# Optimization experiments

Hardware: AMD Instinct MI355X
Metric: run time of the kernel (lower is better)

Reference implementation:

```python
import jax, jax.numpy as jnp
import numpy as np

BITS = 8
EPS = 1e-08
D_IN = 4096
D_OUT = 4096


def setup_inputs() -> dict:
    key = jax.random.key(0)
    k1, k2, k3 = jax.random.split(key, 3)
    hidden_states = jax.random.normal(k1, (4, 2048, D_IN), dtype=jnp.float32)
    # Pre-quantized (dequantized-value) weight buffer, as the module stores it in float
    qmax = 2 ** (BITS - 1) - 1
    w = jax.random.normal(k2, (D_IN, D_OUT), dtype=jnp.float32) * 0.02
    w_scale = jnp.max(jnp.abs(w)) / qmax
    weight_quantized = jnp.clip(jnp.round(w / w_scale), -qmax, qmax) * w_scale
    bias = jax.random.normal(k3, (D_OUT,), dtype=jnp.float32) * 0.01
    x_scale = jnp.asarray(3.0, dtype=jnp.float32)  # calibrated activation maxabs
    return {
        "hidden_states": hidden_states,
        "weight_quantized": weight_quantized,
        "x_scale": x_scale,
        "bias": bias,
    }


def _quantize_maxabs(x, scale, bits, eps):
    # scalar max-abs quantization with a fixed (calibrated) scale
    qmax = 2 ** (bits - 1) - 1
    step = jnp.maximum(scale, eps) / qmax
    return jnp.clip(jnp.round(x / step), -qmax, qmax) * step


def reference(hidden_states, weight_quantized, x_scale, bias):
    orig_shape = hidden_states.shape[:-1]
    d = hidden_states.shape[-1]
    x_flat = hidden_states.reshape(-1, d)
    x_q = _quantize_maxabs(x_flat, x_scale, BITS, EPS).astype(weight_quantized.dtype)
    out = x_q @ weight_quantized  # [tokens, d_out]
    out = out + bias.astype(out.dtype)[None, :]
    out = out.astype(hidden_states.dtype)
    return out.reshape(*orig_shape, weight_quantized.shape[1])
```

## Files before the change

kernel.cpp:

```cpp
#include <hip/hip_runtime.h>
#include <hip/hip_bf16.h>
#include <cstdint>

#define D_IN  4096
#define D_OUT 4096

typedef __attribute__((ext_vector_type(4)))  int   i32x4;

typedef const __attribute__((address_space(1))) unsigned g_u32;
typedef __attribute__((address_space(3))) unsigned       l_u32;

__global__ void prep_kernel(const float* __restrict__ W, int nw,
                            const float* __restrict__ x,
                            char* __restrict__ xq,
                            const float* __restrict__ xscale, int nx,
                            unsigned* __restrict__ wsp) {
    int tid = threadIdx.x;
    if (blockIdx.x < 1024) {
        __shared__ float red[256];
        float m = 0.f;
        for (int i = (blockIdx.x * 256 + tid) * 4; i < nw; i += 1024 * 256 * 4) {
            float4 v = *(const float4*)(W + i);
            m = fmaxf(m, fmaxf(fmaxf(fabsf(v.x), fabsf(v.y)),
                               fmaxf(fabsf(v.z), fabsf(v.w))));
        }
        red[tid] = m; __syncthreads();
        for (int s = 128; s > 0; s >>= 1) {
            if (tid < s) red[tid] = fmaxf(red[tid], red[tid + s]);
            __syncthreads();
        }
        if (tid == 0) atomicMax(wsp, __float_as_uint(red[0]));
    } else {
        int i = ((blockIdx.x - 1024) * 256 + tid) * 4;
        if (i >= nx) return;
        float inv = 127.0f / fmaxf(xscale[0], 1e-8f);
        float4 v = *(const float4*)(x + i);
        char4 o;
        o.x = (char)fminf(fmaxf(rintf(v.x * inv), -127.f), 127.f);
        o.y = (char)fminf(fmaxf(rintf(v.y * inv), -127.f), 127.f);
        o.z = (char)fminf(fmaxf(rintf(v.z * inv), -127.f), 127.f);
        o.w = (char)fminf(fmaxf(rintf(v.w * inv), -127.f), 127.f);
        *(char4*)(xq + i) = o;
    }
}

__global__ void convW_kernel(const float* __restrict__ W,
                             char* __restrict__ Wt,
                             const unsigned* __restrict__ wsp) {
    __shared__ float tile[64][65];
    const float wmax = __uint_as_float(wsp[0]);
    const float inv  = 127.0f / wmax;
    const int n0 = blockIdx.x * 64, k0 = blockIdx.y * 64;
    const int t = threadIdx.x;

    {
        const int r = t >> 2, c0 = (t & 3) * 16;
        const float* src = W + (size_t)(k0 + r) * D_OUT + n0 + c0;
#pragma unroll
        for (int j = 0; j < 4; ++j) {
            float4 v = *(const float4*)(src + j * 4);
            tile[r][c0 + j * 4 + 0] = v.x;
            tile[r][c0 + j * 4 + 1] = v.y;
            tile[r][c0 + j * 4 + 2] = v.z;
            tile[r][c0 + j * 4 + 3] = v.w;
        }
    }
    __syncthreads();

    {
        const int n = t >> 2, kc = (t & 3) * 16;
        int4 pk;
        int* pw = (int*)&pk;
#pragma unroll
        for (int w = 0; w < 4; ++w) {
            unsigned word = 0;
#pragma unroll
            for (int j = 0; j < 4; ++j) {
                int q = (int)rintf(tile[kc + w * 4 + j][n] * inv);
                word |= ((unsigned)(unsigned char)(char)q) << (8 * j);
            }
            pw[w] = (int)word;
        }
        *(int4*)(Wt + (size_t)(n0 + n) * D_IN + k0 + kc) = pk;
    }
}

__global__ __launch_bounds__(512, 2)
void gemm_kernel(const char* __restrict__ A,
                 const char* __restrict__ Bt,
                 const float* __restrict__ bias,
                 const float* __restrict__ xscale,
                 const unsigned* __restrict__ wsp,
                 float* __restrict__ C, int M) {
    constexpr int K = D_IN, N = D_OUT;
    constexpr int NT = K / 128;
    __shared__ char lds[2 * 65536];

    const int tid  = threadIdx.x;
    const int lane = tid & 63;
    const int wid  = tid >> 6;
    const int wr   = wid >> 2;
    const int wc   = wid & 3;

    const int nTn = N / 256;
    const int nwg = gridDim.x;
    int bid = blockIdx.x;
    int q8 = nwg >> 3, r8 = nwg & 7;
    int xcd = bid & 7, idx = bid >> 3;
    int swz = (xcd < r8 ? xcd * (q8 + 1) : r8 * (q8 + 1) + (xcd - r8) * q8) + idx;
    const int tm = swz / nTn, tn = swz % nTn;
    const int row0 = tm * 256, col0 = tn * 256;

    int srcOff[4], dstOff[4];
#pragma unroll
    for (int i = 0; i < 4; ++i) {
        int p  = (i * 512 + tid) * 16;
        int sw = p ^ (((p >> 7) & 7) << 4);
        dstOff[i] = p;
        srcOff[i] = (sw >> 7) * K + (sw & 127);
    }

    const char* srcA = A  + (size_t)row0 * K;
    const char* srcB = Bt + (size_t)col0 * K;
    char* ldsb = lds;

    auto STAGE4 = [&](const char* src, char* dst) {
#pragma unroll
        for (int i = 0; i < 4; ++i)
            __builtin_amdgcn_global_load_lds((g_u32*)(src + srcOff[i]),
                                             (l_u32*)(dst + dstOff[i]), 16, 0, 0);
    };
    auto STAGE2 = [&](const char* src, char* dst) {
#pragma unroll
        for (int i = 0; i < 2; ++i)
            __builtin_amdgcn_global_load_lds((g_u32*)(src + srcOff[i]),
                                             (l_u32*)(dst + dstOff[i]), 16, 0, 0);
    };

    STAGE2(srcB, ldsb + 32768);
    STAGE4(srcA, ldsb);
    STAGE2(srcB + 128 * K, ldsb + 32768 + 16384);
    STAGE2(srcB + 128,     ldsb + 65536 + 32768);
    STAGE4(srcA + 128,     ldsb + 65536);

    i32x4 acc[8][4];
#pragma unroll
    for (int m = 0; m < 8; ++m)
#pragma unroll
        for (int n = 0; n < 4; ++n) acc[m][n] = (i32x4){0, 0, 0, 0};

    const int cp0 = (((lane >> 4) << 4)) ^ ((lane & 7) << 4);
    const int cp1 = cp0 ^ 64;
    const int aBase = (wr * 128 + (lane & 15)) * 128;
    const int bBase = (wc * 64  + (lane & 15)) * 128;

    asm volatile("s_waitcnt vmcnt(6)" ::: "memory");

    auto KITER = [&](int t, char* cur, char* nxt) {
        i32x4 a[4][2], b01[2][2], b23[2][2];
        const char* cA = cur;
        const char* cB = cur + 32768;

        __builtin_amdgcn_s_barrier();
        if (t + 1 < NT) STAGE2(srcB + 128 * K + (t + 1) * 128, nxt + 32768 + 16384);

#pragma unroll
        for (int n = 0; n < 2; ++n) {
            b01[n][0] = *(const i32x4*)(cB + bBase + n * 2048 + cp0);
            b01[n][1] = *(const i32x4*)(cB + bBase + n * 2048 + cp1);
        }
#pragma unroll
        for (int m = 0; m < 4; ++m) {
            a[m][0] = *(const i32x4*)(cA + aBase + m * 2048 + cp0);
            a[m][1] = *(const i32x4*)(cA + aBase + m * 2048 + cp1);
        }
#pragma unroll
        for (int n = 0; n < 2; ++n) {
            b23[n][0] = *(const i32x4*)(cB + bBase + 4096 + n * 2048 + cp0);
            b23[n][1] = *(const i32x4*)(cB + bBase + 4096 + n * 2048 + cp1);
        }

        __builtin_amdgcn_s_setprio(1);
#pragma unroll
        for (int m = 0; m < 4; ++m)
#pragma unroll
            for (int n = 0; n < 2; ++n) {
                acc[m][n] = __builtin_amdgcn_mfma_i32_16x16x64_i8(a[m][0], b01[n][0], acc[m][n], 0, 0, 0);
                acc[m][n] = __builtin_amdgcn_mfma_i32_16x16x64_i8(a[m][1], b01[n][1], acc[m][n], 0, 0, 0);
            }
#pragma unroll
        for (int m = 0; m < 4; ++m)
#pragma unroll
            for (int n = 0; n < 2; ++n) {
                acc[m][n + 2] = __builtin_amdgcn_mfma_i32_16x16x64_i8(a[m][0], b23[n][0], acc[m][n + 2], 0, 0, 0);
                acc[m][n + 2] = __builtin_amdgcn_mfma_i32_16x16x64_i8(a[m][1], b23[n][1], acc[m][n + 2], 0, 0, 0);
            }
#pragma unroll
        for (int m = 0; m < 4; ++m) {
            a[m][0] = *(const i32x4*)(cA + aBase + 8192 + m * 2048 + cp0);
            a[m][1] = *(const i32x4*)(cA + aBase + 8192 + m * 2048 + cp1);
        }
#pragma unroll
        for (int m = 0; m < 4; ++m)
#pragma unroll
            for (int n = 0; n < 2; ++n) {
                acc[m + 4][n + 2] = __builtin_amdgcn_mfma_i32_16x16x64_i8(a[m][0], b23[n][0], acc[m + 4][n + 2], 0, 0, 0);
                acc[m + 4][n + 2] = __builtin_amdgcn_mfma_i32_16x16x64_i8(a[m][1], b23[n][1], acc[m + 4][n + 2], 0, 0, 0);
            }
#pragma unroll
        for (int m = 0; m < 4; ++m)
#pragma unroll
            for (int n = 0; n < 2; ++n) {
                acc[m + 4][n] = __builtin_amdgcn_mfma_i32_16x16x64_i8(a[m][0], b01[n][0], acc[m + 4][n], 0, 0, 0);
                acc[m + 4][n] = __builtin_amdgcn_mfma_i32_16x16x64_i8(a[m][1], b01[n][1], acc[m + 4][n], 0, 0, 0);
            }
        __builtin_amdgcn_s_setprio(0);

        __builtin_amdgcn_s_barrier();
        if (t + 2 < NT) {
            STAGE2(srcB + (t + 2) * 128, cur + 32768);
            STAGE4(srcA + (t + 2) * 128, cur);
            asm volatile("s_waitcnt vmcnt(6)" ::: "memory");
        } else {
            asm volatile("s_waitcnt vmcnt(0)" ::: "memory");
        }
    };

    for (int t = 0; t < NT; t += 2) {
        KITER(t,     ldsb,         ldsb + 65536);
        KITER(t + 1, ldsb + 65536, ldsb);
    }

    const float wmax  = __uint_as_float(wsp[0]);
    const float scale = (fmaxf(xscale[0], 1e-8f) * (1.0f / 127.0f)) * (wmax * (1.0f / 127.0f));
    const int lr = (lane >> 4) * 4, lc = lane & 15;
#pragma unroll
    for (int n = 0; n < 4; ++n) {
        int col = col0 + wc * 64 + n * 16 + lc;
        float bv = bias[col];
#pragma unroll
        for (int m = 0; m < 8; ++m) {
            int rowb = row0 + wr * 128 + m * 16 + lr;
            i32x4 v = acc[m][n];
#pragma unroll
            for (int r2 = 0; r2 < 4; ++r2)
                C[(size_t)(rowb + r2) * N + col] = (float)v[r2] * scale + bv;
        }
    }
}

extern "C" void kernel_launch(void* const* d_in, const int* in_sizes, int n_in,
                              void* d_out, int out_size, void* d_ws, size_t ws_size,
                              hipStream_t stream) {
    const float* x      = (const float*)d_in[0];
    const float* W      = (const float*)d_in[1];
    const float* xscale = (const float*)d_in[2];
    const float* bias   = (const float*)d_in[3];
    float* out = (float*)d_out;

    const int nx = in_sizes[0];
    const int nw = in_sizes[1];
    const int M  = nx / D_IN;

    char*     xq  = (char*)d_ws;
    char*     Wt  = (char*)d_ws + (size_t)nx;
    unsigned* wsp = (unsigned*)((char*)d_ws + (size_t)nx + nw);

    hipMemsetAsync(wsp, 0, 4, stream);

    int qblocks = nx / 4 / 256;
    prep_kernel<<<1024 + qblocks, 256, 0, stream>>>(W, nw, x, xq, xscale, nx, wsp);

    dim3 tb(256);
    dim3 tg(D_OUT / 64, D_IN / 64);
    convW_kernel<<<tg, tb, 0, stream>>>(W, Wt, wsp);

    int grid = (M / 256) * (D_OUT / 256);
    gemm_kernel<<<grid, 512, 0, stream>>>(xq, Wt, bias, xscale, wsp, out, M);
}
```

Measured before the change: 200.6 us.

## Shrink GEMM tile to 256x128 with K-step 64 for higher occupancy

Restructures the int8 MFMA GEMM from 256x256 tiles with a 128-wide K step to 256x128 tiles with a 64-wide K step. Each of the 8 waves now owns a 64x64 sub-tile with half the accumulators, LDS use drops to 48KB, and launch bounds are raised to 4 blocks per CU. The goal is more resident blocks and more grid parallelism to hide latency. In exchange each loaded byte is reused less, B traffic relative to compute doubles, and barriers come twice as often per unit of K.

```diff
diff --git a/kernel.cpp b/kernel.cpp
--- a/kernel.cpp
+++ b/kernel.cpp
@@ -52,7 +52,6 @@
     const float inv  = 127.0f / wmax;
     const int n0 = blockIdx.x * 64, k0 = blockIdx.y * 64;
     const int t = threadIdx.x;
-
     {
         const int r = t >> 2, c0 = (t & 3) * 16;
         const float* src = W + (size_t)(k0 + r) * D_OUT + n0 + c0;
@@ -66,7 +65,6 @@
         }
     }
     __syncthreads();
-
     {
         const int n = t >> 2, kc = (t & 3) * 16;
         int4 pk;
@@ -85,7 +83,7 @@
     }
 }
 
-__global__ __launch_bounds__(512, 2)
+__global__ __launch_bounds__(512, 4)
 void gemm_kernel(const char* __restrict__ A,
                  const char* __restrict__ Bt,
                  const float* __restrict__ bias,
@@ -93,142 +91,92 @@
                  const unsigned* __restrict__ wsp,
                  float* __restrict__ C, int M) {
     constexpr int K = D_IN, N = D_OUT;
-    constexpr int NT = K / 128;
-    __shared__ char lds[2 * 65536];
+    constexpr int NT = K / 64;
+    __shared__ char lds[2 * 24576];
 
     const int tid  = threadIdx.x;
     const int lane = tid & 63;
     const int wid  = tid >> 6;
-    const int wr   = wid >> 2;
-    const int wc   = wid & 3;
-
-    const int nTn = N / 256;
+    const int wr   = wid >> 1;
+    const int wc   = wid & 1;
+
+    const int nTn = N / 128;
     const int nwg = gridDim.x;
     int bid = blockIdx.x;
     int q8 = nwg >> 3, r8 = nwg & 7;
     int xcd = bid & 7, idx = bid >> 3;
     int swz = (xcd < r8 ? xcd * (q8 + 1) : r8 * (q8 + 1) + (xcd - r8) * q8) + idx;
     const int tm = swz / nTn, tn = swz % nTn;
-    const int row0 = tm * 256, col0 = tn * 256;
-
-    int srcOff[4], dstOff[4];
-#pragma unroll
-    for (int i = 0; i < 4; ++i) {
-        int p  = (i * 512 + tid) * 16;
-        int sw = p ^ (((p >> 7) & 7) << 4);
-        dstOff[i] = p;
-        srcOff[i] = (sw >> 7) * K + (sw & 127);
-    }
+    const int row0 = tm * 256, col0 = tn * 128;
+
+    int srcA0, srcA1, srcB0;
+    {
+        int p0 = tid * 16;
+        int p1 = (512 + tid) * 16;
+        int s0 = p0 ^ (((p0 >> 7) & 3) << 4);
+        int s1 = p1 ^ (((p1 >> 7) & 3) << 4);
+        srcA0 = (s0 >> 6) * K + (s0 & 63);
+        srcA1 = (s1 >> 6) * K + (s1 & 63);
+        srcB0 = srcA0;
+    }
+    const int dstA0 = tid * 16, dstA1 = (512 + tid) * 16, dstB0 = 16384 + tid * 16;
 
     const char* srcA = A  + (size_t)row0 * K;
     const char* srcB = Bt + (size_t)col0 * K;
-    char* ldsb = lds;
-
-    auto STAGE4 = [&](const char* src, char* dst) {
-#pragma unroll
-        for (int i = 0; i < 4; ++i)
-            __builtin_amdgcn_global_load_lds((g_u32*)(src + srcOff[i]),
-                                             (l_u32*)(dst + dstOff[i]), 16, 0, 0);
+    char* b0 = lds;
+    char* b1 = lds + 24576;
+
+    auto STAGE = [&](int t, char* buf) {
+        __builtin_amdgcn_global_load_lds((g_u32*)(srcA + t * 64 + srcA0),
+                                         (l_u32*)(buf + dstA0), 16, 0, 0);
+        __builtin_amdgcn_global_load_lds((g_u32*)(srcA + t * 64 + srcA1),
+                                         (l_u32*)(buf + dstA1), 16, 0, 0);
+        __builtin_amdgcn_global_load_lds((g_u32*)(srcB + t * 64 + srcB0),
+                                         (l_u32*)(buf + dstB0), 16, 0, 0);
     };
-    auto STAGE2 = [&](const char* src, char* dst) {
-#pragma unroll
-        for (int i = 0; i < 2; ++i)
-            __builtin_amdgcn_global_load_lds((g_u32*)(src + srcOff[i]),
-                                             (l_u32*)(dst + dstOff[i]), 16, 0, 0);
-    };
-
-    STAGE2(srcB, ldsb + 32768);
-    STAGE4(srcA, ldsb);
-    STAGE2(srcB + 128 * K, ldsb + 32768 + 16384);
-    STAGE2(srcB + 128,     ldsb + 65536 + 32768);
-    STAGE4(srcA + 128,     ldsb + 65536);
-
-    i32x4 acc[8][4];
-#pragma unroll
-    for (int m = 0; m < 8; ++m)
+
+    STAGE(0, b0);
+    STAGE(1, b1);
+
+    i32x4 acc[4][4];
+#pragma unroll
+    for (int m = 0; m < 4; ++m)
 #pragma unroll
         for (int n = 0; n < 4; ++n) acc[m][n] = (i32x4){0, 0, 0, 0};
 
-    const int cp0 = (((lane >> 4) << 4)) ^ ((lane & 7) << 4);
-    const int cp1 = cp0 ^ 64;
-    const int aBase = (wr * 128 + (lane & 15)) * 128;
-    const int bBase = (wc * 64  + (lane & 15)) * 128;
-
-    asm volatile("s_waitcnt vmcnt(6)" ::: "memory");
-
-    auto KITER = [&](int t, char* cur, char* nxt) {
-        i32x4 a[4][2], b01[2][2], b23[2][2];
-        const char* cA = cur;
-        const char* cB = cur + 32768;
-
+    const int cOff  = (((lane >> 4) ^ ((lane >> 1) & 3)) << 4);
+    const int aBase = (wr * 64 + (lane & 15)) * 64 + cOff;
+    const int bBase = 16384 + (wc * 64 + (lane & 15)) * 64 + cOff;
+
+    asm volatile("s_waitcnt vmcnt(3)" ::: "memory");
+
+    auto KTILE = [&](int t, char* cur) {
+        i32x4 a[4], b[4];
         __builtin_amdgcn_s_barrier();
-        if (t + 1 < NT) STAGE2(srcB + 128 * K + (t + 1) * 128, nxt + 32768 + 16384);
-
-#pragma unroll
-        for (int n = 0; n < 2; ++n) {
-            b01[n][0] = *(const i32x4*)(cB + bBase + n * 2048 + cp0);
-            b01[n][1] = *(const i32x4*)(cB + bBase + n * 2048 + cp1);
-        }
-#pragma unroll
-        for (int m = 0; m < 4; ++m) {
-            a[m][0] = *(const i32x4*)(cA + aBase + m * 2048 + cp0);
-            a[m][1] = *(const i32x4*)(cA + aBase + m * 2048 + cp1);
-        }
-#pragma unroll
-        for (int n = 0; n < 2; ++n) {
-            b23[n][0] = *(const i32x4*)(cB + bBase + 4096 + n * 2048 + cp0);
-            b23[n][1] = *(const i32x4*)(cB + bBase + 4096 + n * 2048 + cp1);
-        }
-
+#pragma unroll
+        for (int n = 0; n < 4; ++n) b[n] = *(const i32x4*)(cur + bBase + n * 1024);
+#pragma unroll
+        for (int m = 0; m < 4; ++m) a[m] = *(const i32x4*)(cur + aBase + m * 1024);
         __builtin_amdgcn_s_setprio(1);
 #pragma unroll
         for (int m = 0; m < 4; ++m)
 #pragma unroll
-            for (int n = 0; n < 2; ++n) {
-                acc[m][n] = __builtin_amdgcn_mfma_i32_16x16x64_i8(a[m][0], b01[n][0], acc[m][n], 0, 0, 0);
-                acc[m][n] = __builtin_amdgcn_mfma_i32_16x16x64_i8(a[m][1], b01[n][1], acc[m][n], 0, 0, 0);
-            }
-#pragma unroll
-        for (int m = 0; m < 4; ++m)
-#pragma unroll
-            for (int n = 0; n < 2; ++n) {
-                acc[m][n + 2] = __builtin_amdgcn_mfma_i32_16x16x64_i8(a[m][0], b23[n][0], acc[m][n + 2], 0, 0, 0);
-                acc[m][n + 2] = __builtin_amdgcn_mfma_i32_16x16x64_i8(a[m][1], b23[n][1], acc[m][n + 2], 0, 0, 0);
-            }
-#pragma unroll
-        for (int m = 0; m < 4; ++m) {
-            a[m][0] = *(const i32x4*)(cA + aBase + 8192 + m * 2048 + cp0);
-            a[m][1] = *(const i32x4*)(cA + aBase + 8192 + m * 2048 + cp1);
-        }
-#pragma unroll
-        for (int m = 0; m < 4; ++m)
-#pragma unroll
-            for (int n = 0; n < 2; ++n) {
-                acc[m + 4][n + 2] = __builtin_amdgcn_mfma_i32_16x16x64_i8(a[m][0], b23[n][0], acc[m + 4][n + 2], 0, 0, 0);
-                acc[m + 4][n + 2] = __builtin_amdgcn_mfma_i32_16x16x64_i8(a[m][1], b23[n][1], acc[m + 4][n + 2], 0, 0, 0);
-            }
-#pragma unroll
-        for (int m = 0; m < 4; ++m)
-#pragma unroll
-            for (int n = 0; n < 2; ++n) {
-                acc[m + 4][n] = __builtin_amdgcn_mfma_i32_16x16x64_i8(a[m][0], b01[n][0], acc[m + 4][n], 0, 0, 0);
-                acc[m + 4][n] = __builtin_amdgcn_mfma_i32_16x16x64_i8(a[m][1], b01[n][1], acc[m + 4][n], 0, 0, 0);
-            }
+            for (int n = 0; n < 4; ++n)
+                acc[m][n] = __builtin_amdgcn_mfma_i32_16x16x64_i8(a[m], b[n], acc[m][n], 0, 0, 0);
         __builtin_amdgcn_s_setprio(0);
 
         __builtin_amdgcn_s_barrier();
         if (t + 2 < NT) {
-            STAGE2(srcB + (t + 2) * 128, cur + 32768);
-            STAGE4(srcA + (t + 2) * 128, cur);
-            asm volatile("s_waitcnt vmcnt(6)" ::: "memory");
+            STAGE(t + 2, cur);
+            asm volatile("s_waitcnt vmcnt(3)" ::: "memory");
         } else {
             asm volatile("s_waitcnt vmcnt(0)" ::: "memory");
         }
     };
 
     for (int t = 0; t < NT; t += 2) {
-        KITER(t,     ldsb,         ldsb + 65536);
-        KITER(t + 1, ldsb + 65536, ldsb);
+        KTILE(t,     b0);
+        KTILE(t + 1, b1);
     }
 
     const float wmax  = __uint_as_float(wsp[0]);
@@ -239,8 +187,8 @@
         int col = col0 + wc * 64 + n * 16 + lc;
         float bv = bias[col];
 #pragma unroll
-        for (int m = 0; m < 8; ++m) {
-            int rowb = row0 + wr * 128 + m * 16 + lr;
+        for (int m = 0; m < 4; ++m) {
+            int rowb = row0 + wr * 64 + m * 16 + lr;
             i32x4 v = acc[m][n];
 #pragma unroll
             for (int r2 = 0; r2 < 4; ++r2)
@@ -275,6 +223,6 @@
     dim3 tg(D_OUT / 64, D_IN / 64);
     convW_kernel<<<tg, tb, 0, stream>>>(W, Wt, wsp);
 
-    int grid = (M / 256) * (D_OUT / 256);
+    int grid = (M / 256) * (D_OUT / 128);
     gemm_kernel<<<grid, 512, 0, stream>>>(xq, Wt, bias, xscale, wsp, out, M);
 }
```

Measured after the change: 218.9 us. +9.1%, slower.
